# Kernel optimization log

Hardware: AMD Instinct MI355X
Metric: run time of the kernel (lower is better)

## Reference

```python
import jax, jax.numpy as jnp
import numpy as np

N0, N1, N2 = 65536, 8192, 1024   # node counts per depth (pool factor 8, as in original m1*2=8)
DEG = 6                          # avg degree of k-space neighbor graphs
K = 10                           # number of Gaussian kernels in GMMConv


def _pool_graph(n_fine):
    # bidirectional edges between each group of 8 nodes and its representative (last node of group)
    mem = jnp.arange(n_fine)
    rep = (mem // 8) * 8 + 7
    return jnp.concatenate([mem, rep]), jnp.concatenate([rep, mem])


def setup_inputs() -> dict:
    key = jax.random.key(0)
    ks = list(jax.random.split(key, 40))
    E1, E2, E3 = DEG * N0, DEG * N1, DEG * N2
    d = {}
    d['n_feat'] = jax.random.normal(ks[0], (N0, 2), jnp.float32)
    d['src1'] = jax.random.randint(ks[1], (E1,), 0, N0)
    d['dst1'] = jax.random.randint(ks[2], (E1,), 0, N0)
    d['pkor1'] = 0.5 * jax.random.normal(ks[3], (E1, 2), jnp.float32)
    d['src2'] = jax.random.randint(ks[4], (E2,), 0, N1)
    d['dst2'] = jax.random.randint(ks[5], (E2,), 0, N1)
    d['pkor2'] = 0.5 * jax.random.normal(ks[6], (E2, 2), jnp.float32)
    d['src3'] = jax.random.randint(ks[7], (E3,), 0, N2)
    d['dst3'] = jax.random.randint(ks[8], (E3,), 0, N2)
    d['pkor3'] = 0.5 * jax.random.normal(ks[9], (E3, 2), jnp.float32)
    d['pm1_src'], d['pm1_dst'] = _pool_graph(N0)
    d['pm2_src'], d['pm2_dst'] = _pool_graph(N1)
    d['idx1'] = jnp.arange(N1) * 8 + 7
    d['idx2'] = jnp.arange(N2) * 8 + 7

    def lin(k, fi, fo):
        return jax.random.normal(k, (fi, K * fo), jnp.float32) / np.float32(np.sqrt(fi * K))

    d['W1'] = lin(ks[10], 2, 32)
    d['mu1'] = jax.random.normal(ks[11], (K, 2), jnp.float32)
    d['is1'] = jax.random.uniform(ks[12], (K, 2), jnp.float32, 0.5, 1.5)
    d['b1'] = 0.01 * jax.random.normal(ks[13], (32,), jnp.float32)
    d['W2'] = lin(ks[14], 32, 64)
    d['mu2'] = jax.random.normal(ks[15], (K, 2), jnp.float32)
    d['is2'] = jax.random.uniform(ks[16], (K, 2), jnp.float32, 0.5, 1.5)
    d['W3'] = lin(ks[17], 64, 128)
    d['mu3'] = jax.random.normal(ks[18], (K, 2), jnp.float32)
    d['is3'] = jax.random.uniform(ks[19], (K, 2), jnp.float32, 0.5, 1.5)
    d['W4'] = lin(ks[20], 192, 64)
    d['mu4'] = jax.random.normal(ks[21], (K, 2), jnp.float32)
    d['is4'] = jax.random.uniform(ks[22], (K, 2), jnp.float32, 0.5, 1.5)
    d['W5'] = lin(ks[23], 96, 40)
    d['mu5'] = jax.random.normal(ks[24], (K, 2), jnp.float32)
    d['is5'] = jax.random.uniform(ks[25], (K, 2), jnp.float32, 0.5, 1.5)
    d['b5'] = 0.01 * jax.random.normal(ks[26], (40,), jnp.float32)
    return d


def gmm_conv(x, W, mu, inv_sigma, src, dst, pseudo, n, bias=None):
    # DGL GMMConv, aggregator 'mean': h=fc(x) -> (N,K,F); gaussian edge weights over 2D pseudo coords
    h = (x @ W).reshape(x.shape[0], K, -1)                                   # (N,K,F)
    diff = pseudo[:, None, :] - mu[None, :, :]                               # (E,K,2)
    gw = jnp.exp(-0.5 * jnp.sum(diff * diff * (inv_sigma[None] ** 2), -1))   # (E,K)
    msg = h[src] * gw[:, :, None]                                            # (E,K,F)
    s = jax.ops.segment_sum(msg, dst, num_segments=n)
    deg = jax.ops.segment_sum(jnp.ones(dst.shape, x.dtype), dst, num_segments=n)
    out = jnp.sum(s / jnp.maximum(deg, 1.0)[:, None, None], axis=1)          # mean over edges, sum over kernels
    return out if bias is None else out + bias


def max_reduce(h, src, dst, n):
    # DGL update_all(copy_u, max): nodes with no in-edges get 0
    m = jax.ops.segment_max(h[src], dst, num_segments=n)
    deg = jax.ops.segment_sum(jnp.ones(dst.shape, h.dtype), dst, num_segments=n)
    return jnp.where(deg[:, None] > 0, m, jnp.zeros((), h.dtype))


def reference(n_feat, src1, dst1, pkor1, src2, dst2, pkor2, src3, dst3, pkor3,
              pm1_src, pm1_dst, pm2_src, pm2_dst, idx1, idx2,
              W1, mu1, is1, b1, W2, mu2, is2, W3, mu3, is3,
              W4, mu4, is4, W5, mu5, is5, b5):
    # encoder
    out0 = jax.nn.relu(gmm_conv(n_feat, W1, mu1, is1, src1, dst1, pkor1, N0, b1))      # (N0,32) skip0
    h = max_reduce(out0, pm1_src, pm1_dst, N0)[idx1]                                    # MaxPool -> (N1,32)
    out1 = jax.nn.relu(gmm_conv(h, W2, mu2, is2, src2, dst2, pkor2, N1))                # (N1,64) skip1
    h = max_reduce(out1, pm2_src, pm2_dst, N1)[idx2]                                    # MaxPool -> (N2,64)
    out2 = jax.nn.relu(gmm_conv(h, W3, mu3, is3, src3, dst3, pkor3, N2))                # (N2,128) bottleneck
    # decoder
    hu = jnp.zeros((N1, out2.shape[1]), out2.dtype).at[idx2].set(out2)
    hu = max_reduce(hu, pm2_src, pm2_dst, N1)                                           # UpSample -> (N1,128)
    out3 = jax.nn.relu(gmm_conv(jnp.concatenate([hu, out1], 1), W4, mu4, is4,
                                src2, dst2, pkor2, N1))                                 # (N1,64)
    hu = jnp.zeros((N0, out3.shape[1]), out3.dtype).at[idx1].set(out3)
    hu = max_reduce(hu, pm1_src, pm1_dst, N0)                                           # UpSample -> (N0,64)
    return jnp.tanh(gmm_conv(jnp.concatenate([hu, out0], 1), W5, mu5, is5,
                             src1, dst1, pkor1, N0, b5))                                # (N0,40)
```

## Files before the change

kernel.cpp:

```cpp
#include <hip/hip_runtime.h>


#define N0C 65536
#define N1C 8192
#define N2C 1024
#define KK 10

typedef _Float16 half2t __attribute__((ext_vector_type(2)));
typedef _Float16 half4 __attribute__((ext_vector_type(4)));
typedef _Float16 f16x8 __attribute__((ext_vector_type(8)));
typedef float f32x4 __attribute__((ext_vector_type(4)));

static inline int cdiv(long long a, long long b) { return (int)((a + b - 1) / b); }

__device__ __forceinline__ size_t fragi(int r, int kd, int KDT) {
    return ((size_t)(r >> 4) * KDT + (kd >> 5)) * 64 + ((kd >> 3) & 3) * 16 + (r & 15);
}


__global__ __launch_bounds__(256)
void k_hist3(const int* __restrict__ d1, const int* __restrict__ d2,
             const int* __restrict__ d3, int* __restrict__ g1,
             int* __restrict__ g2, int* __restrict__ g3,
             int E1, int E2, int E3) {
    int i = blockIdx.x * 256 + threadIdx.x;
    if (i < E1) atomicAdd(&g1[d1[i]], 1);
    else if (i < E1 + E2) atomicAdd(&g2[d2[i - E1]], 1);
    else if (i < E1 + E2 + E3) atomicAdd(&g3[d3[i - E1 - E2]], 1);
}

__device__ __forceinline__ void map_graph(int b, int& lb, int& gi) {
    if (b < 256) { gi = 0; lb = b; }
    else if (b < 288) { gi = 1; lb = b - 256; }
    else { gi = 2; lb = b - 288; }
}

__global__ __launch_bounds__(256)
void k_scan1_3(const int* __restrict__ deg1, int* __restrict__ off1,
               const int* __restrict__ deg2, int* __restrict__ off2,
               const int* __restrict__ deg3, int* __restrict__ off3,
               int* __restrict__ part) {
    __shared__ int s[256];
    int lb, gi; map_graph(blockIdx.x, lb, gi);
    const int* deg = gi == 0 ? deg1 : (gi == 1 ? deg2 : deg3);
    int* off = gi == 0 ? off1 : (gi == 1 ? off2 : off3);
    int* prt = part + (gi == 0 ? 0 : (gi == 1 ? 256 : 288));
    int i = lb * 256 + threadIdx.x;
    int v = deg[i];
    s[threadIdx.x] = v;
    __syncthreads();
#pragma unroll
    for (int d = 1; d < 256; d <<= 1) {
        int t = (threadIdx.x >= d) ? s[threadIdx.x - d] : 0;
        __syncthreads();
        s[threadIdx.x] += t;
        __syncthreads();
    }
    off[i] = s[threadIdx.x] - v;
    if (threadIdx.x == 255) prt[lb] = s[255];
}

__global__ __launch_bounds__(256)
void k_scan2_3(int* __restrict__ part) {
    __shared__ int s[256];
    int nb = blockIdx.x == 0 ? 256 : (blockIdx.x == 1 ? 32 : 4);
    int* p = part + (blockIdx.x == 0 ? 0 : (blockIdx.x == 1 ? 256 : 288));
    int v = (threadIdx.x < nb) ? p[threadIdx.x] : 0;
    s[threadIdx.x] = v;
    __syncthreads();
#pragma unroll
    for (int d = 1; d < 256; d <<= 1) {
        int t = (threadIdx.x >= d) ? s[threadIdx.x - d] : 0;
        __syncthreads();
        s[threadIdx.x] += t;
        __syncthreads();
    }
    if (threadIdx.x < nb) p[threadIdx.x] = s[threadIdx.x] - v;
}

__global__ __launch_bounds__(256)
void k_scan3_3(int* __restrict__ off1, int* __restrict__ off2, int* __restrict__ off3,
               const int* __restrict__ part,
               const int* __restrict__ deg1, const int* __restrict__ deg2,
               const int* __restrict__ deg3,
               float* __restrict__ inv1, float* __restrict__ inv2,
               float* __restrict__ inv3, int E1, int E2, int E3) {
    int lb, gi; map_graph(blockIdx.x, lb, gi);
    int* off = gi == 0 ? off1 : (gi == 1 ? off2 : off3);
    const int* deg = gi == 0 ? deg1 : (gi == 1 ? deg2 : deg3);
    float* inv = gi == 0 ? inv1 : (gi == 1 ? inv2 : inv3);
    const int* prt = part + (gi == 0 ? 0 : (gi == 1 ? 256 : 288));
    int n = gi == 0 ? N0C : (gi == 1 ? N1C : N2C);
    int E = gi == 0 ? E1 : (gi == 1 ? E2 : E3);
    int i = lb * 256 + threadIdx.x;
    off[i] += prt[lb];
    inv[i] = 1.0f / fmaxf((float)deg[i], 1.0f);
    if (i == n - 1) off[n] = E;
}

__global__ __launch_bounds__(256)
void k_scatter3(const int* __restrict__ s1, const int* __restrict__ d1,
                const float* __restrict__ p1, const int* __restrict__ o1,
                int* __restrict__ c1, int* __restrict__ cs1, float2* __restrict__ cp1,
                const int* __restrict__ s2, const int* __restrict__ d2,
                const float* __restrict__ p2, const int* __restrict__ o2,
                int* __restrict__ c2, int* __restrict__ cs2, float2* __restrict__ cp2,
                const int* __restrict__ s3, const int* __restrict__ d3,
                const float* __restrict__ p3, const int* __restrict__ o3,
                int* __restrict__ c3, int* __restrict__ cs3, float2* __restrict__ cp3,
                int E1, int E2, int E3) {
    int i = blockIdx.x * 256 + threadIdx.x;
    const int* src; const int* dst; const float* pk; const int* off;
    int* cur; int* csrc; float2* cpk; int e;
    if (i < E1) { src = s1; dst = d1; pk = p1; off = o1; cur = c1; csrc = cs1; cpk = cp1; e = i; }
    else if (i < E1 + E2) { src = s2; dst = d2; pk = p2; off = o2; cur = c2; csrc = cs2; cpk = cp2; e = i - E1; }
    else if (i < E1 + E2 + E3) { src = s3; dst = d3; pk = p3; off = o3; cur = c3; csrc = cs3; cpk = cp3; e = i - E1 - E2; }
    else return;
    int d = dst[e];
    int p = off[d] + atomicAdd(&cur[d], 1);
    csrc[p] = src[e];
    cpk[p] = reinterpret_cast<const float2*>(pk)[e];
}

__global__ __launch_bounds__(256)
void k_gw(const float2* __restrict__ cp1, const float2* __restrict__ cp2,
          const float2* __restrict__ cp3,
          const float* __restrict__ mu1, const float* __restrict__ is1,
          const float* __restrict__ mu5, const float* __restrict__ is5,
          const float* __restrict__ mu2, const float* __restrict__ is2,
          const float* __restrict__ mu4, const float* __restrict__ is4,
          const float* __restrict__ mu3, const float* __restrict__ is3,
          float* __restrict__ g1, float* __restrict__ g5, float* __restrict__ g2,
          float* __restrict__ g4, float* __restrict__ g3,
          int E1, int E2, int E3) {
    int i = blockIdx.x * 256 + threadIdx.x;
    const float2* cp; const float* mu; const float* isg; float* g; int e;
    if (i < E1) { cp = cp1; mu = mu1; isg = is1; g = g1; e = i; }
    else if (i < 2 * E1) { cp = cp1; mu = mu5; isg = is5; g = g5; e = i - E1; }
    else if (i < 2 * E1 + E2) { cp = cp2; mu = mu2; isg = is2; g = g2; e = i - 2 * E1; }
    else if (i < 2 * E1 + 2 * E2) { cp = cp2; mu = mu4; isg = is4; g = g4; e = i - 2 * E1 - E2; }
    else if (i < 2 * E1 + 2 * E2 + E3) { cp = cp3; mu = mu3; isg = is3; g = g3; e = i - 2 * E1 - 2 * E2; }
    else return;
    float2 pk = cp[e];
    float o[KK];
#pragma unroll
    for (int k = 0; k < KK; ++k) {
        float dx = (pk.x - mu[2 * k]) * isg[2 * k];
        float dy = (pk.y - mu[2 * k + 1]) * isg[2 * k + 1];
        o[k] = __expf(-0.5f * (dx * dx + dy * dy));
    }
    float4* gp = reinterpret_cast<float4*>(g + (size_t)e * 12);
    gp[0] = make_float4(o[0], o[1], o[2], o[3]);
    gp[1] = make_float4(o[4], o[5], o[6], o[7]);
    gp[2] = make_float4(o[8], o[9], 0.f, 0.f);
}

#define LOAD_G(gw, j, G)                                                     \
    float G[KK];                                                             \
    {                                                                        \
        const float4* gp_ = reinterpret_cast<const float4*>((gw) + (size_t)(j) * 12); \
        float4 g0_ = gp_[0], g1_ = gp_[1]; float2 g2_ = *reinterpret_cast<const float2*>(gp_ + 2); \
        G[0] = g0_.x; G[1] = g0_.y; G[2] = g0_.z; G[3] = g0_.w;              \
        G[4] = g1_.x; G[5] = g1_.y; G[6] = g1_.z; G[7] = g1_.w;              \
        G[8] = g2_.x; G[9] = g2_.y;                                          \
    }

__global__ __launch_bounds__(256)
void k_prep_wt(const float* __restrict__ W1, const float* __restrict__ W2,
               const float* __restrict__ W3, const float* __restrict__ W4,
               const float* __restrict__ W5,
               _Float16* __restrict__ T2,
               _Float16* __restrict__ T3, _Float16* __restrict__ T4,
               _Float16* __restrict__ T5) {
    int id = blockIdx.x * 256 + threadIdx.x;
    if (id < 20480) {
        int f = id / 320, kc = id % 320;
        T2[fragi(f, kc, 10) * 8 + (kc & 7)] = (_Float16)W2[(kc % 32) * 640 + (kc / 32) * 64 + f];
        return;
    }
    id -= 20480;
    if (id < 81920) {
        int f = id / 640, kc = id % 640;
        T3[fragi(f, kc, 20) * 8 + (kc & 7)] = (_Float16)W3[(kc % 64) * 1280 + (kc / 64) * 128 + f];
        return;
    }
    id -= 81920;
    if (id < 122880) {
        int f = id / 1920, kc = id % 1920;
        T4[fragi(f, kc, 60) * 8 + (kc & 7)] = (_Float16)W4[(kc % 192) * 640 + (kc / 192) * 64 + f];
        return;
    }
    id -= 122880;
    if (id < 46080) {
        int f = id / 960, kc = id % 960;
        float v = (f < 40) ? W5[(kc % 96) * 400 + (kc / 96) * 40 + f] : 0.0f;
        T5[fragi(f, kc, 30) * 8 + (kc & 7)] = (_Float16)v;
    }
}

__global__ __launch_bounds__(256, 3)
void k_l1(const float* __restrict__ x, const int* __restrict__ off,
          const int* __restrict__ csrc, const float* __restrict__ gw,
          const float* __restrict__ inv, const float* __restrict__ W1,
          const float* __restrict__ b1, _Float16* __restrict__ out0) {
    __shared__ float Ws[640];
    __shared__ float bs[32];
    for (int i = threadIdx.x; i < 640; i += 256) Ws[i] = W1[i];
    if (threadIdx.x < 32) bs[threadIdx.x] = b1[threadIdx.x];
    __syncthreads();
    int n = blockIdx.x * 256 + threadIdx.x;
    float a0[KK], a1[KK];
#pragma unroll
    for (int k = 0; k < KK; ++k) { a0[k] = 0.f; a1[k] = 0.f; }
    int j0 = off[n], j1 = off[n + 1];
    int j = j0;
    for (; j + 1 < j1; j += 2) {
        int sa = csrc[j];
        int sb = csrc[j + 1];
        LOAD_G(gw, j, Ga)
        LOAD_G(gw, j + 1, Gb)
        float2 xa = reinterpret_cast<const float2*>(x)[sa];
        float2 xb = reinterpret_cast<const float2*>(x)[sb];
#pragma unroll
        for (int k = 0; k < KK; ++k) {
            a0[k] = fmaf(Ga[k], xa.x, a0[k]);
            a1[k] = fmaf(Ga[k], xa.y, a1[k]);
            a0[k] = fmaf(Gb[k], xb.x, a0[k]);
            a1[k] = fmaf(Gb[k], xb.y, a1[k]);
        }
    }
    if (j < j1) {
        int sa = csrc[j];
        LOAD_G(gw, j, Ga)
        float2 xa = reinterpret_cast<const float2*>(x)[sa];
#pragma unroll
        for (int k = 0; k < KK; ++k) {
            a0[k] = fmaf(Ga[k], xa.x, a0[k]);
            a1[k] = fmaf(Ga[k], xa.y, a1[k]);
        }
    }
    float iv = inv[n];
#pragma unroll
    for (int k = 0; k < KK; ++k) { a0[k] *= iv; a1[k] *= iv; }
    _Float16* orow = out0 + (size_t)n * 32;
#pragma unroll
    for (int f4 = 0; f4 < 8; ++f4) {
        float v0 = bs[f4 * 4], v1 = bs[f4 * 4 + 1], v2 = bs[f4 * 4 + 2], v3 = bs[f4 * 4 + 3];
#pragma unroll
        for (int k = 0; k < KK; ++k) {
            const float* w0 = Ws + k * 32 + f4 * 4;
            const float* w1 = w0 + 320;
            v0 += a0[k] * w0[0] + a1[k] * w1[0];
            v1 += a0[k] * w0[1] + a1[k] * w1[1];
            v2 += a0[k] * w0[2] + a1[k] * w1[2];
            v3 += a0[k] * w0[3] + a1[k] * w1[3];
        }
        half4 o;
        o[0] = (_Float16)fmaxf(v0, 0.f); o[1] = (_Float16)fmaxf(v1, 0.f);
        o[2] = (_Float16)fmaxf(v2, 0.f); o[3] = (_Float16)fmaxf(v3, 0.f);
        *reinterpret_cast<half4*>(orow + f4 * 4) = o;
    }
}

template <int TPN>
__global__ __launch_bounds__(256, 3)
void k_aggx(const _Float16* __restrict__ xp, const int* __restrict__ off,
            const int* __restrict__ csrc, const float* __restrict__ gw,
            const float* __restrict__ inv, _Float16* __restrict__ agg, int N) {
    constexpr int CIN = TPN * 4;
    constexpr int KDT = KK * CIN / 32;
    int tid = threadIdx.x;
    int nl = tid / TPN, tt = tid - nl * TPN;
    int node = blockIdx.x * (256 / TPN) + nl;
    if (node >= N) return;
    float a[KK][4];
#pragma unroll
    for (int k = 0; k < KK; ++k)
#pragma unroll
        for (int e = 0; e < 4; ++e) a[k][e] = 0.f;
    int j0 = off[node], j1 = off[node + 1];
    int j = j0;
    for (; j + 1 < j1; j += 2) {
        int sa = csrc[j];
        int sb = csrc[j + 1];
        LOAD_G(gw, j, Ga)
        LOAD_G(gw, j + 1, Gb)
        half4 ha = *reinterpret_cast<const half4*>(xp + (size_t)sa * CIN + 4 * tt);
        half4 hb = *reinterpret_cast<const half4*>(xp + (size_t)sb * CIN + 4 * tt);
        float a0 = ha[0], a1 = ha[1], a2 = ha[2], a3 = ha[3];
        float b0 = hb[0], b1 = hb[1], b2 = hb[2], b3 = hb[3];
#pragma unroll
        for (int k = 0; k < KK; ++k) {
            a[k][0] = fmaf(Ga[k], a0, a[k][0]);
            a[k][1] = fmaf(Ga[k], a1, a[k][1]);
            a[k][2] = fmaf(Ga[k], a2, a[k][2]);
            a[k][3] = fmaf(Ga[k], a3, a[k][3]);
            a[k][0] = fmaf(Gb[k], b0, a[k][0]);
            a[k][1] = fmaf(Gb[k], b1, a[k][1]);
            a[k][2] = fmaf(Gb[k], b2, a[k][2]);
            a[k][3] = fmaf(Gb[k], b3, a[k][3]);
        }
    }
    if (j < j1) {
        int sa = csrc[j];
        LOAD_G(gw, j, Ga)
        half4 ha = *reinterpret_cast<const half4*>(xp + (size_t)sa * CIN + 4 * tt);
        float a0 = ha[0], a1 = ha[1], a2 = ha[2], a3 = ha[3];
#pragma unroll
        for (int k = 0; k < KK; ++k) {
            a[k][0] = fmaf(Ga[k], a0, a[k][0]);
            a[k][1] = fmaf(Ga[k], a1, a[k][1]);
            a[k][2] = fmaf(Ga[k], a2, a[k][2]);
            a[k][3] = fmaf(Ga[k], a3, a[k][3]);
        }
    }
    float iv = inv[node];
#pragma unroll
    for (int k = 0; k < KK; ++k) {
        half4 o;
        o[0] = (_Float16)(a[k][0] * iv); o[1] = (_Float16)(a[k][1] * iv);
        o[2] = (_Float16)(a[k][2] * iv); o[3] = (_Float16)(a[k][3] * iv);
        int kd = k * CIN + 4 * tt;
        *reinterpret_cast<half4*>(agg + fragi(node, kd, KDT) * 8 + (kd & 7)) = o;
    }
}

template <int CA, int CB, int WPB, int NPW>
__global__ __launch_bounds__(WPB * 64)
void k_aggf3(const _Float16* __restrict__ xA, const _Float16* __restrict__ xB,
             const int* __restrict__ off, const int* __restrict__ csrc,
             const float* __restrict__ gw, const float* __restrict__ inv,
             _Float16* __restrict__ agg, int nodeBase) {
    constexpr int CIN = CA + CB;
    constexpr int PAIRS = CIN / 2;
    constexpr int P = (PAIRS + 63) / 64;
    constexpr int KDT = KK * CIN / 32;
    constexpr int STRIDE = KK * CIN + 8;
    __shared__ _Float16 lds[16 * STRIDE];
    const int lane = threadIdx.x & 63;
    const int wv = threadIdx.x >> 6;
#pragma unroll
    for (int u = 0; u < NPW; ++u) {
        const int nl = wv * NPW + u;
        const int node = __builtin_amdgcn_readfirstlane(nodeBase + blockIdx.x * 16 + nl);
        float a[KK][2 * P];
#pragma unroll
        for (int k = 0; k < KK; ++k)
#pragma unroll
            for (int p = 0; p < 2 * P; ++p) a[k][p] = 0.f;
        int j0 = __builtin_amdgcn_readfirstlane(off[node]);
        int j1 = __builtin_amdgcn_readfirstlane(off[node + 1]);
        int deg = j1 - j0;
        if (deg > 0) {
            int pl = j0 + (lane < deg ? lane : deg - 1);
            int sall = csrc[pl];
            int e = 0;
            for (; e + 1 < deg; e += 2) {
                int sa = __builtin_amdgcn_readlane(sall, e);
                int sb = __builtin_amdgcn_readlane(sall, e + 1);
                LOAD_G(gw, j0 + e, Ga)
                LOAD_G(gw, j0 + e + 1, Gb)
                float xa0[P], xa1[P], xb0[P], xb1[P];
#pragma unroll
                for (int p = 0; p < P; ++p) {
                    int c0 = 2 * (lane + 64 * p);
                    xa0[p] = 0.f; xa1[p] = 0.f; xb0[p] = 0.f; xb1[p] = 0.f;
                    if (c0 < CIN) {
                        const _Float16* qa = (c0 < CA) ? (xA + (size_t)(sa >> 3) * CA + c0)
                                                       : (xB + (size_t)sa * CB + (c0 - CA));
                        const _Float16* qb = (c0 < CA) ? (xA + (size_t)(sb >> 3) * CA + c0)
                                                       : (xB + (size_t)sb * CB + (c0 - CA));
                        half2t ha = *reinterpret_cast<const half2t*>(qa);
                        half2t hb = *reinterpret_cast<const half2t*>(qb);
                        xa0[p] = ha[0]; xa1[p] = ha[1];
                        xb0[p] = hb[0]; xb1[p] = hb[1];
                    }
                }
#pragma unroll
                for (int k = 0; k < KK; ++k)
#pragma unroll
                    for (int p = 0; p < P; ++p) {
                        a[k][2 * p] = fmaf(Ga[k], xa0[p], a[k][2 * p]);
                        a[k][2 * p + 1] = fmaf(Ga[k], xa1[p], a[k][2 * p + 1]);
                        a[k][2 * p] = fmaf(Gb[k], xb0[p], a[k][2 * p]);
                        a[k][2 * p + 1] = fmaf(Gb[k], xb1[p], a[k][2 * p + 1]);
                    }
            }
            if (e < deg) {
                int sa = __builtin_amdgcn_readlane(sall, e);
                LOAD_G(gw, j0 + e, Ga)
                float xa0[P], xa1[P];
#pragma unroll
                for (int p = 0; p < P; ++p) {
                    int c0 = 2 * (lane + 64 * p);
                    xa0[p] = 0.f; xa1[p] = 0.f;
                    if (c0 < CIN) {
                        const _Float16* qa = (c0 < CA) ? (xA + (size_t)(sa >> 3) * CA + c0)
                                                       : (xB + (size_t)sa * CB + (c0 - CA));
                        half2t ha = *reinterpret_cast<const half2t*>(qa);
                        xa0[p] = ha[0]; xa1[p] = ha[1];
                    }
                }
#pragma unroll
                for (int k = 0; k < KK; ++k)
#pragma unroll
                    for (int p = 0; p < P; ++p) {
                        a[k][2 * p] = fmaf(Ga[k], xa0[p], a[k][2 * p]);
                        a[k][2 * p + 1] = fmaf(Ga[k], xa1[p], a[k][2 * p + 1]);
                    }
            }
        }
        float iv = inv[node];
#pragma unroll
        for (int k = 0; k < KK; ++k)
#pragma unroll
            for (int p = 0; p < P; ++p) {
                int c0 = 2 * (lane + 64 * p);
                if (c0 < CIN) {
                    half2t o;
                    o[0] = (_Float16)(a[k][2 * p] * iv);
                    o[1] = (_Float16)(a[k][2 * p + 1] * iv);
                    *reinterpret_cast<half2t*>(&lds[nl * STRIDE + k * CIN + c0]) = o;
                }
            }
    }
    __syncthreads();
    f16x8* ag = reinterpret_cast<f16x8*>(agg);
    for (int s = threadIdx.x; s < KDT * 64; s += WPB * 64) {
        int t = s >> 6, l = s & 63;
        int nd = l & 15, q = l >> 4;
        f16x8 v = *reinterpret_cast<const f16x8*>(&lds[nd * STRIDE + t * 32 + q * 8]);
        ag[((size_t)blockIdx.x * KDT + t) * 64 + l] = v;
    }
}

template <int WB, int NT, int ITERS, int KS, int ACT, int FST, int OUTH>
__global__ __launch_bounds__(WB * 64)
void k_gemm2(const _Float16* __restrict__ A, const _Float16* __restrict__ B,
             const float* __restrict__ bias, void* __restrict__ outv, int M) {
    constexpr int KDT = KS * ITERS;
    constexpr int F = NT * 16;
    const int lane = threadIdx.x & 63;
    const int wv = threadIdx.x >> 6;
    const int lm = lane & 15;
    const int q = lane >> 4;
    const int ks = blockIdx.x;
    const int t0 = ks * ITERS;
    const size_t m0 = (size_t)blockIdx.y * (WB * 16) + wv * 16;
    const size_t mblk = m0 >> 4;
    f32x4 acc[NT];
#pragma unroll
    for (int t = 0; t < NT; ++t) acc[t] = (f32x4){0.f, 0.f, 0.f, 0.f};
    const f16x8* ap = (const f16x8*)A + (mblk * KDT + t0) * 64 + lane;
    const f16x8* bp = (const f16x8*)B + (size_t)t0 * 64 + lane;
    f16x8 af = ap[0];
    f16x8 bf[NT];
#pragma unroll
    for (int t = 0; t < NT; ++t) bf[t] = bp[(size_t)t * KDT * 64];
#pragma unroll
    for (int i = 0; i < ITERS; ++i) {
        f16x8 afn; f16x8 bfn[NT];
        if (i + 1 < ITERS) {
            afn = ap[(size_t)(i + 1) * 64];
#pragma unroll
            for (int t = 0; t < NT; ++t)
                bfn[t] = bp[((size_t)t * KDT + i + 1) * 64];
        }
#pragma unroll
        for (int t = 0; t < NT; ++t)
            acc[t] = __builtin_amdgcn_mfma_f32_16x16x32_f16(af, bf[t], acc[t], 0, 0, 0);
        af = afn;
#pragma unroll
        for (int t = 0; t < NT; ++t) bf[t] = bfn[t];
    }
    if (KS == 1) {
#pragma unroll
        for (int t = 0; t < NT; ++t) {
            int f = t * 16 + lm;
            if (f < FST) {
                float b = bias ? bias[f] : 0.0f;
#pragma unroll
                for (int r = 0; r < 4; ++r) {
                    float v = acc[t][r] + b;
                    v = (ACT == 1) ? tanhf(v) : fmaxf(v, 0.0f);
                    if (OUTH) ((_Float16*)outv)[(m0 + q * 4 + r) * (size_t)FST + f] = (_Float16)v;
                    else ((float*)outv)[(m0 + q * 4 + r) * (size_t)FST + f] = v;
                }
            }
        }
    } else {
        float* pout = (float*)outv + (size_t)ks * M * F;
#pragma unroll
        for (int t = 0; t < NT; ++t) {
            int f = t * 16 + lm;
#pragma unroll
            for (int r = 0; r < 4; ++r)
                pout[(m0 + q * 4 + r) * (size_t)F + f] = acc[t][r];
        }
    }
}

template <int KS, int F, int FST, int ACT, int OUTH>
__global__ __launch_bounds__(256)
void k_redact(const float* __restrict__ part, const float* __restrict__ bias,
              void* __restrict__ outv, int M) {
    int i = blockIdx.x * 256 + threadIdx.x;
    if (i >= M * FST) return;
    int m = i / FST, f = i - m * FST;
    float v = 0.0f;
#pragma unroll
    for (int s = 0; s < KS; ++s) v += part[((size_t)s * M + m) * F + f];
    if (bias) v += bias[f];
    v = (ACT == 1) ? tanhf(v) : fmaxf(v, 0.0f);
    if (OUTH) ((_Float16*)outv)[(size_t)m * FST + f] = (_Float16)v;
    else ((float*)outv)[(size_t)m * FST + f] = v;
}

__global__ __launch_bounds__(256)
void k_pool8h(const _Float16* __restrict__ in, _Float16* __restrict__ out, int total, int F) {
    int i = blockIdx.x * 256 + threadIdx.x;
    if (i >= total) return;
    int j = i / F;
    int f = i - j * F;
    const _Float16* p = in + (size_t)(j << 3) * F + f;
    float m = (float)p[0];
#pragma unroll
    for (int r = 1; r < 8; ++r) m = fmaxf(m, (float)p[(size_t)r * F]);
    out[i] = (_Float16)m;
}

extern "C" void kernel_launch(void* const* d_in, const int* in_sizes, int n_in,
                              void* d_out, int out_size, void* d_ws, size_t ws_size,
                              hipStream_t stream) {
    const float* n_feat = (const float*)d_in[0];
    const int* src1 = (const int*)d_in[1];
    const int* dst1 = (const int*)d_in[2];
    const float* pkor1 = (const float*)d_in[3];
    const int* src2 = (const int*)d_in[4];
    const int* dst2 = (const int*)d_in[5];
    const float* pkor2 = (const float*)d_in[6];
    const int* src3 = (const int*)d_in[7];
    const int* dst3 = (const int*)d_in[8];
    const float* pkor3 = (const float*)d_in[9];
    const float* W1 = (const float*)d_in[16];
    const float* mu1 = (const float*)d_in[17];
    const float* is1 = (const float*)d_in[18];
    const float* b1 = (const float*)d_in[19];
    const float* W2 = (const float*)d_in[20];
    const float* mu2 = (const float*)d_in[21];
    const float* is2 = (const float*)d_in[22];
    const float* W3 = (const float*)d_in[23];
    const float* mu3 = (const float*)d_in[24];
    const float* is3 = (const float*)d_in[25];
    const float* W4 = (const float*)d_in[26];
    const float* mu4 = (const float*)d_in[27];
    const float* is4 = (const float*)d_in[28];
    const float* W5 = (const float*)d_in[29];
    const float* mu5 = (const float*)d_in[30];
    const float* is5 = (const float*)d_in[31];
    const float* b5 = (const float*)d_in[32];

    const int E1 = in_sizes[1], E2 = in_sizes[4], E3 = in_sizes[7];
    const int NT_ = N0C + N1C + N2C;

    char* w = (char*)d_ws;
    auto alloc = [&](size_t bytes) {
        void* p = (void*)w;
        w += (bytes + 255) & ~(size_t)255;
        return p;
    };
    int* degs = (int*)alloc((size_t)NT_ * 2 * 4);
    int* deg1 = degs, *deg2 = degs + N0C, *deg3 = degs + N0C + N1C;
    int* cur1 = degs + NT_, *cur2 = cur1 + N0C, *cur3 = cur2 + N1C;
    int* off1 = (int*)alloc(((size_t)N0C + 1) * 4);
    int* off2 = (int*)alloc(((size_t)N1C + 1) * 4);
    int* off3 = (int*)alloc(((size_t)N2C + 1) * 4);
    int* part = (int*)alloc(292 * 4);
    int* csrc1 = (int*)alloc((size_t)E1 * 4);
    float2* cpk1 = (float2*)alloc((size_t)E1 * 8);
    int* csrc2 = (int*)alloc((size_t)E2 * 4);
    float2* cpk2 = (float2*)alloc((size_t)E2 * 8);
    int* csrc3 = (int*)alloc((size_t)E3 * 4);
    float2* cpk3 = (float2*)alloc((size_t)E3 * 8);
    float* inv1 = (float*)alloc((size_t)N0C * 4);
    float* inv2 = (float*)alloc((size_t)N1C * 4);
    float* inv3 = (float*)alloc((size_t)N2C * 4);
    float* g1 = (float*)alloc(((size_t)2 * E1 + 2 * E2 + E3) * 12 * 4);
    float* g5 = g1 + (size_t)E1 * 12;
    float* g2 = g5 + (size_t)E1 * 12;
    float* g4 = g2 + (size_t)E2 * 12;
    float* g3 = g4 + (size_t)E2 * 12;
    _Float16* out0 = (_Float16*)alloc((size_t)N0C * 32 * 2);
    _Float16* out1 = (_Float16*)alloc((size_t)N1C * 64 * 2);
    _Float16* out2 = (_Float16*)alloc((size_t)N2C * 128 * 2);
    _Float16* out3 = (_Float16*)alloc((size_t)N1C * 64 * 2);
    _Float16* hp1 = (_Float16*)alloc((size_t)N1C * 32 * 2);
    _Float16* hp2 = (_Float16*)alloc((size_t)N2C * 64 * 2);
    _Float16* agg2 = (_Float16*)alloc((size_t)N1C * 320 * 2);
    _Float16* agg3 = (_Float16*)alloc((size_t)N2C * 640 * 2);
    _Float16* Wt2 = (_Float16*)alloc((size_t)64 * 320 * 2);
    _Float16* Wt3 = (_Float16*)alloc((size_t)128 * 640 * 2);
    _Float16* Wt4 = (_Float16*)alloc((size_t)64 * 1920 * 2);
    _Float16* Wt5 = (_Float16*)alloc((size_t)48 * 960 * 2);
    size_t used = (size_t)(w - (char*)d_ws);
    size_t rem = (ws_size > used) ? (ws_size - used) : 0;
    _Float16* agg4 = (_Float16*)w;
    float* part4 = (float*)(w + (((size_t)N1C * 1920 * 2 + 255) & ~(size_t)255));
    int npass = 1;
    while ((size_t)(N0C / npass) * 1920 > rem && npass < 16) npass <<= 1;
    const int chunk = N0C / npass;
    _Float16* agg5 = (_Float16*)w;

    const int ET = E1 + E2 + E3;
    const int GT = 2 * E1 + 2 * E2 + E3;

    hipMemsetAsync(degs, 0, (size_t)NT_ * 2 * 4, stream);
    k_prep_wt<<<cdiv(271360, 256), 256, 0, stream>>>(W1, W2, W3, W4, W5,
                                                     Wt2, Wt3, Wt4, Wt5);
    k_hist3<<<cdiv(ET, 256), 256, 0, stream>>>(dst1, dst2, dst3, deg1, deg2, deg3, E1, E2, E3);
    k_scan1_3<<<292, 256, 0, stream>>>(deg1, off1, deg2, off2, deg3, off3, part);
    k_scan2_3<<<3, 256, 0, stream>>>(part);
    k_scan3_3<<<292, 256, 0, stream>>>(off1, off2, off3, part, deg1, deg2, deg3,
                                       inv1, inv2, inv3, E1, E2, E3);
    k_scatter3<<<cdiv(ET, 256), 256, 0, stream>>>(
        src1, dst1, pkor1, off1, cur1, csrc1, cpk1,
        src2, dst2, pkor2, off2, cur2, csrc2, cpk2,
        src3, dst3, pkor3, off3, cur3, csrc3, cpk3, E1, E2, E3);
    k_gw<<<cdiv(GT, 256), 256, 0, stream>>>(
        cpk1, cpk2, cpk3, mu1, is1, mu5, is5, mu2, is2, mu4, is4, mu3, is3,
        g1, g5, g2, g4, g3, E1, E2, E3);

    k_l1<<<N0C / 256, 256, 0, stream>>>(n_feat, off1, csrc1, g1, inv1, W1, b1, out0);

    k_pool8h<<<cdiv(N1C * 32, 256), 256, 0, stream>>>(out0, hp1, N1C * 32, 32);
    k_aggx<8><<<cdiv(N1C, 32), 256, 0, stream>>>(hp1, off2, csrc2, g2, inv2, agg2, N1C);
    k_gemm2<2, 4, 10, 1, 0, 64, 1><<<dim3(1, N1C / 32), 128, 0, stream>>>(agg2, Wt2, nullptr, out1, N1C);

    k_pool8h<<<cdiv(N2C * 64, 256), 256, 0, stream>>>(out1, hp2, N2C * 64, 64);
    k_aggx<16><<<cdiv(N2C, 16), 256, 0, stream>>>(hp2, off3, csrc3, g3, inv3, agg3, N2C);
    k_gemm2<1, 8, 20, 1, 0, 128, 1><<<dim3(1, N2C / 16), 64, 0, stream>>>(agg3, Wt3, nullptr, out2, N2C);

    k_aggf3<128, 64, 16, 1><<<N1C / 16, 1024, 0, stream>>>(
        out2, out1, off2, csrc2, g4, inv2, agg4, 0);
    k_gemm2<2, 4, 15, 4, 0, 64, 0><<<dim3(4, N1C / 32), 128, 0, stream>>>(agg4, Wt4, nullptr, part4, N1C);
    k_redact<4, 64, 64, 0, 1><<<cdiv(N1C * 64, 256), 256, 0, stream>>>(part4, nullptr, out3, N1C);

    for (int p = 0; p < npass; ++p) {
        int base = p * chunk;
        k_aggf3<64, 32, 8, 2><<<chunk / 16, 512, 0, stream>>>(
            out3, out0, off1, csrc1, g5, inv1, agg5, base);
        k_gemm2<4, 3, 30, 1, 1, 40, 0><<<dim3(1, chunk / 64), 256, 0, stream>>>(
            agg5, Wt5, b5, ((float*)d_out) + (size_t)base * 40, chunk);
    }
}
```

Before: 343.9 us.

## Fuse decoder aggregation with MFMA GEMM epilogue, dropping global agg buffers

```diff
diff --git a/kernel.cpp b/kernel.cpp
--- a/kernel.cpp
+++ b/kernel.cpp
@@ -325,12 +325,13 @@
     }
 }
 
-template <int CA, int CB, int WPB, int NPW>
+template <int CA, int CB, int WPB, int NPW, int NT, int ACT, int FST, int OUTH>
 __global__ __launch_bounds__(WPB * 64)
-void k_aggf3(const _Float16* __restrict__ xA, const _Float16* __restrict__ xB,
+void k_aggf4(const _Float16* __restrict__ xA, const _Float16* __restrict__ xB,
              const int* __restrict__ off, const int* __restrict__ csrc,
              const float* __restrict__ gw, const float* __restrict__ inv,
-             _Float16* __restrict__ agg, int nodeBase) {
+             const _Float16* __restrict__ Wt, const float* __restrict__ bias,
+             void* __restrict__ outv, int nodeBase) {
     constexpr int CIN = CA + CB;
     constexpr int PAIRS = CIN / 2;
     constexpr int P = (PAIRS + 63) / 64;
@@ -425,34 +426,54 @@
             }
     }
     __syncthreads();
-    f16x8* ag = reinterpret_cast<f16x8*>(agg);
-    for (int s = threadIdx.x; s < KDT * 64; s += WPB * 64) {
-        int t = s >> 6, l = s & 63;
-        int nd = l & 15, q = l >> 4;
-        f16x8 v = *reinterpret_cast<const f16x8*>(&lds[nd * STRIDE + t * 32 + q * 8]);
-        ag[((size_t)blockIdx.x * KDT + t) * 64 + l] = v;
-    }
-}
-
-template <int WB, int NT, int ITERS, int KS, int ACT, int FST, int OUTH>
+    if (wv < NT) {
+        const int lm = lane & 15;
+        const int q = lane >> 4;
+        f32x4 acc = (f32x4){0.f, 0.f, 0.f, 0.f};
+        const f16x8* bp = (const f16x8*)Wt + (size_t)wv * KDT * 64 + lane;
+        f16x8 af = *reinterpret_cast<const f16x8*>(&lds[lm * STRIDE + q * 8]);
+        f16x8 bf = bp[0];
+#pragma unroll
+        for (int i = 0; i < KDT; ++i) {
+            f16x8 afn, bfn;
+            if (i + 1 < KDT) {
+                afn = *reinterpret_cast<const f16x8*>(&lds[lm * STRIDE + (i + 1) * 32 + q * 8]);
+                bfn = bp[(size_t)(i + 1) * 64];
+            }
+            acc = __builtin_amdgcn_mfma_f32_16x16x32_f16(af, bf, acc, 0, 0, 0);
+            af = afn; bf = bfn;
+        }
+        int f = wv * 16 + lm;
+        if (f < FST) {
+            float b = bias ? bias[f] : 0.0f;
+#pragma unroll
+            for (int r = 0; r < 4; ++r) {
+                size_t node = (size_t)nodeBase + (size_t)blockIdx.x * 16 + q * 4 + r;
+                float v = acc[r] + b;
+                v = (ACT == 1) ? tanhf(v) : fmaxf(v, 0.0f);
+                if (OUTH) ((_Float16*)outv)[node * FST + f] = (_Float16)v;
+                else ((float*)outv)[node * FST + f] = v;
+            }
+        }
+    }
+}
+
+template <int WB, int NT, int ITERS, int ACT, int FST, int OUTH>
 __global__ __launch_bounds__(WB * 64)
 void k_gemm2(const _Float16* __restrict__ A, const _Float16* __restrict__ B,
              const float* __restrict__ bias, void* __restrict__ outv, int M) {
-    constexpr int KDT = KS * ITERS;
-    constexpr int F = NT * 16;
+    constexpr int KDT = ITERS;
     const int lane = threadIdx.x & 63;
     const int wv = threadIdx.x >> 6;
     const int lm = lane & 15;
     const int q = lane >> 4;
-    const int ks = blockIdx.x;
-    const int t0 = ks * ITERS;
     const size_t m0 = (size_t)blockIdx.y * (WB * 16) + wv * 16;
     const size_t mblk = m0 >> 4;
     f32x4 acc[NT];
 #pragma unroll
     for (int t = 0; t < NT; ++t) acc[t] = (f32x4){0.f, 0.f, 0.f, 0.f};
-    const f16x8* ap = (const f16x8*)A + (mblk * KDT + t0) * 64 + lane;
-    const f16x8* bp = (const f16x8*)B + (size_t)t0 * 64 + lane;
+    const f16x8* ap = (const f16x8*)A + mblk * KDT * 64 + lane;
+    const f16x8* bp = (const f16x8*)B + lane;
     f16x8 af = ap[0];
     f16x8 bf[NT];
 #pragma unroll
@@ -473,47 +494,20 @@
 #pragma unroll
         for (int t = 0; t < NT; ++t) bf[t] = bfn[t];
     }
-    if (KS == 1) {
-#pragma unroll
-        for (int t = 0; t < NT; ++t) {
-            int f = t * 16 + lm;
-            if (f < FST) {
-                float b = bias ? bias[f] : 0.0f;
-#pragma unroll
-                for (int r = 0; r < 4; ++r) {
-                    float v = acc[t][r] + b;
-                    v = (ACT == 1) ? tanhf(v) : fmaxf(v, 0.0f);
-                    if (OUTH) ((_Float16*)outv)[(m0 + q * 4 + r) * (size_t)FST + f] = (_Float16)v;
-                    else ((float*)outv)[(m0 + q * 4 + r) * (size_t)FST + f] = v;
-                }
+#pragma unroll
+    for (int t = 0; t < NT; ++t) {
+        int f = t * 16 + lm;
+        if (f < FST) {
+            float b = bias ? bias[f] : 0.0f;
+#pragma unroll
+            for (int r = 0; r < 4; ++r) {
+                float v = acc[t][r] + b;
+                v = (ACT == 1) ? tanhf(v) : fmaxf(v, 0.0f);
+                if (OUTH) ((_Float16*)outv)[(m0 + q * 4 + r) * (size_t)FST + f] = (_Float16)v;
+                else ((float*)outv)[(m0 + q * 4 + r) * (size_t)FST + f] = v;
             }
         }
-    } else {
-        float* pout = (float*)outv + (size_t)ks * M * F;
-#pragma unroll
-        for (int t = 0; t < NT; ++t) {
-            int f = t * 16 + lm;
-#pragma unroll
-            for (int r = 0; r < 4; ++r)
-                pout[(m0 + q * 4 + r) * (size_t)F + f] = acc[t][r];
-        }
-    }
-}
-
-template <int KS, int F, int FST, int ACT, int OUTH>
-__global__ __launch_bounds__(256)
-void k_redact(const float* __restrict__ part, const float* __restrict__ bias,
-              void* __restrict__ outv, int M) {
-    int i = blockIdx.x * 256 + threadIdx.x;
-    if (i >= M * FST) return;
-    int m = i / FST, f = i - m * FST;
-    float v = 0.0f;
-#pragma unroll
-    for (int s = 0; s < KS; ++s) v += part[((size_t)s * M + m) * F + f];
-    if (bias) v += bias[f];
-    v = (ACT == 1) ? tanhf(v) : fmaxf(v, 0.0f);
-    if (OUTH) ((_Float16*)outv)[(size_t)m * FST + f] = (_Float16)v;
-    else ((float*)outv)[(size_t)m * FST + f] = v;
+    }
 }
 
 __global__ __launch_bounds__(256)
@@ -602,14 +596,6 @@
     _Float16* Wt3 = (_Float16*)alloc((size_t)128 * 640 * 2);
     _Float16* Wt4 = (_Float16*)alloc((size_t)64 * 1920 * 2);
     _Float16* Wt5 = (_Float16*)alloc((size_t)48 * 960 * 2);
-    size_t used = (size_t)(w - (char*)d_ws);
-    size_t rem = (ws_size > used) ? (ws_size - used) : 0;
-    _Float16* agg4 = (_Float16*)w;
-    float* part4 = (float*)(w + (((size_t)N1C * 1920 * 2 + 255) & ~(size_t)255));
-    int npass = 1;
-    while ((size_t)(N0C / npass) * 1920 > rem && npass < 16) npass <<= 1;
-    const int chunk = N0C / npass;
-    _Float16* agg5 = (_Float16*)w;
 
     const int ET = E1 + E2 + E3;
     const int GT = 2 * E1 + 2 * E2 + E3;
@@ -634,22 +620,15 @@
 
     k_pool8h<<<cdiv(N1C * 32, 256), 256, 0, stream>>>(out0, hp1, N1C * 32, 32);
     k_aggx<8><<<cdiv(N1C, 32), 256, 0, stream>>>(hp1, off2, csrc2, g2, inv2, agg2, N1C);
-    k_gemm2<2, 4, 10, 1, 0, 64, 1><<<dim3(1, N1C / 32), 128, 0, stream>>>(agg2, Wt2, nullptr, out1, N1C);
+    k_gemm2<2, 4, 10, 0, 64, 1><<<dim3(1, N1C / 32), 128, 0, stream>>>(agg2, Wt2, nullptr, out1, N1C);
 
     k_pool8h<<<cdiv(N2C * 64, 256), 256, 0, stream>>>(out1, hp2, N2C * 64, 64);
     k_aggx<16><<<cdiv(N2C, 16), 256, 0, stream>>>(hp2, off3, csrc3, g3, inv3, agg3, N2C);
-    k_gemm2<1, 8, 20, 1, 0, 128, 1><<<dim3(1, N2C / 16), 64, 0, stream>>>(agg3, Wt3, nullptr, out2, N2C);
-
-    k_aggf3<128, 64, 16, 1><<<N1C / 16, 1024, 0, stream>>>(
-        out2, out1, off2, csrc2, g4, inv2, agg4, 0);
-    k_gemm2<2, 4, 15, 4, 0, 64, 0><<<dim3(4, N1C / 32), 128, 0, stream>>>(agg4, Wt4, nullptr, part4, N1C);
-    k_redact<4, 64, 64, 0, 1><<<cdiv(N1C * 64, 256), 256, 0, stream>>>(part4, nullptr, out3, N1C);
-
-    for (int p = 0; p < npass; ++p) {
-        int base = p * chunk;
-        k_aggf3<64, 32, 8, 2><<<chunk / 16, 512, 0, stream>>>(
-            out3, out0, off1, csrc1, g5, inv1, agg5, base);
-        k_gemm2<4, 3, 30, 1, 1, 40, 0><<<dim3(1, chunk / 64), 256, 0, stream>>>(
-            agg5, Wt5, b5, ((float*)d_out) + (size_t)base * 40, chunk);
-    }
-}
+    k_gemm2<1, 8, 20, 0, 128, 1><<<dim3(1, N2C / 16), 64, 0, stream>>>(agg3, Wt3, nullptr, out2, N2C);
+
+    k_aggf4<128, 64, 16, 1, 4, 0, 64, 1><<<N1C / 16, 1024, 0, stream>>>(
+        out2, out1, off2, csrc2, g4, inv2, Wt4, nullptr, out3, 0);
+
+    k_aggf4<64, 32, 8, 2, 3, 1, 40, 0><<<N0C / 16, 512, 0, stream>>>(
+        out3, out0, off1, csrc1, g5, inv1, Wt5, b5, d_out, 0);
+}
```

Result: faster. 309.8 us (median of 3 runs) (-9.9%).
